# Kernel optimization log

Measured on AMD Instinct MI355X. Metric: run time of the kernel, lower is better.

## Reference

```python
import jax, jax.numpy as jnp
import numpy as np

BS, SL, H, DH = 2, 2048, 32, 128
STRIDE = 16
NUM_PAGES = BS * (SL // STRIDE)  # 256, distinct page per block
PAGE_DIM = 1 * 2 * STRIDE * H * DH  # blocks * partitions * stride * kv_heads * head_dim


def setup_inputs() -> dict:
    key = jax.random.key(0)
    k1, k2, k3 = jax.random.split(key, 3)
    xq = jax.random.normal(k1, (BS, SL, H, DH), dtype=jnp.float32)
    xk = jax.random.normal(k2, (BS, SL, H, DH), dtype=jnp.float32)
    xv = jax.random.normal(k3, (BS, SL, H, DH), dtype=jnp.float32)
    cache_state = jnp.zeros((NUM_PAGES, PAGE_DIM), dtype=jnp.float32)
    seq_block_ids = jnp.arange(BS * (SL // STRIDE), dtype=jnp.int64 if jax.config.jax_enable_x64 else jnp.int32).reshape(BS, SL // STRIDE)
    return {"xq": xq, "xk": xk, "xv": xv, "cache_state": cache_state, "seq_block_ids": seq_block_ids}


def reference(xq, xk, xv, cache_state, seq_block_ids):
    bs, sl, h, dh = xq.shape
    nb = sl // STRIDE  # blocks per sequence
    num_pages = cache_state.shape[0]

    # --- paged cache write (prefill path: start_positions is None) ---
    # page layout: [page, transformer_block(=1), partition(k=0,v=1), stride, head, head_dim]
    cache = cache_state.reshape(num_pages, 1, 2, STRIDE, h, dh)
    pids = seq_block_ids.reshape(-1)  # [bs*nb]
    k_blocks = xk.reshape(bs * nb, STRIDE, h, dh)
    v_blocks = xv.reshape(bs * nb, STRIDE, h, dh)
    cache = cache.at[pids, 0, 0].set(k_blocks)
    cache = cache.at[pids, 0, 1].set(v_blocks)
    new_cache_state = cache.reshape(cache_state.shape)

    # --- GQA repeat_kv: n_rep = head_count // head_count_kv = 1 -> no-op ---

    # --- SDPA, attn_mask=None, is_causal=False ---
    scale = 1.0 / np.sqrt(dh).astype(np.float32)
    scores = jnp.einsum("bqhd,bkhd->bhqk", xq, xk) * scale  # [bs, h, sl, sl]
    attn = jax.nn.softmax(scores, axis=-1)
    out = jnp.einsum("bhqk,bkhd->bqhd", attn, xv)
    attn_output = out.reshape(bs, sl, h * dh)
    return attn_output, new_cache_state
```

## Files before the change

### kernel.cpp

```cpp
#include <hip/hip_runtime.h>
#include <hip/hip_bf16.h>
#include <stdint.h>

#define BS 2
#define SL 2048
#define H 32
#define DH 128
#define ATT_ELEMS (BS*SL*H*DH)
#define KTILES (SL/64)
#define KT32 (SL/32)
#define QSCALE (0.08838834764831845f * 1.4426950408889634f)

typedef __attribute__((ext_vector_type(8))) short short8_t;
typedef __attribute__((ext_vector_type(16))) float f32x16_t;
typedef __attribute__((ext_vector_type(4))) unsigned int u32x4_t;
typedef __attribute__((ext_vector_type(2))) unsigned int u32x2_t;

union FragU { u32x4_t u; short8_t s; };

__device__ __forceinline__ unsigned short f2bf(float x){
    union { float f; unsigned int u; } v; v.f = x;
    unsigned int r = v.u + 0x7fffu + ((v.u >> 16) & 1u);
    return (unsigned short)(r >> 16);
}
__device__ __forceinline__ unsigned int pack2(float a, float b){
    return (unsigned int)f2bf(a) | ((unsigned int)f2bf(b) << 16);
}
__device__ __forceinline__ unsigned int cvtpk(float a, float b){
    unsigned int r;
    asm("v_cvt_pk_bf16_f32 %0, %1, %2" : "=v"(r) : "v"(a), "v"(b));
    return r;
}
__device__ __forceinline__ void gload16(const unsigned short* g, unsigned short* l){
    __builtin_amdgcn_global_load_lds(
        (const __attribute__((address_space(1))) void*)(const void*)g,
        (__attribute__((address_space(3))) void*)(void*)l, 16, 0, 0);
}

__global__ __launch_bounds__(256) void prep_kv_kernel(const float* __restrict__ xk,
                                                      const float* __restrict__ xv,
                                                      const int* __restrict__ pids,
                                                      unsigned short* __restrict__ kfr,
                                                      unsigned short* __restrict__ vfr,
                                                      float* __restrict__ out_cache,
                                                      int do_cache){
    __shared__ unsigned short tK[64*136];
    __shared__ unsigned short tV[64*136];
    int tile = blockIdx.x, h = blockIdx.y, b = blockIdx.z;
    int tid = threadIdx.x;
    size_t tb = ((size_t)((b*H + h)*KTILES + tile)) * 8192;
    int pg[4];
    #pragma unroll
    for (int j = 0; j < 4; ++j) pg[j] = pids[b*128 + tile*4 + j];

    #pragma unroll
    for (int i = 0; i < 8; ++i){
        int c = tid + 256*i;
        int row = c >> 5, f4 = c & 31;
        size_t gidx = ((size_t)((b*SL + tile*64 + row)*H + h))*DH + f4*4;
        float4 kx = *(const float4*)(xk + gidx);
        float4 vx = *(const float4*)(xv + gidx);
        u32x2_t kw; kw[0] = pack2(kx.x, kx.y); kw[1] = pack2(kx.z, kx.w);
        u32x2_t vw; vw[0] = pack2(vx.x, vx.y); vw[1] = pack2(vx.z, vx.w);
        *(u32x2_t*)(&tK[row*136 + f4*4]) = kw;
        *(u32x2_t*)(&tV[row*136 + f4*4]) = vw;
        if (do_cache){
            size_t cb = (size_t)pg[row>>4]*131072 + (size_t)(row&15)*4096 + h*128 + f4*4;
            *(float4*)(out_cache + cb)         = kx;
            *(float4*)(out_cache + cb + 65536) = vx;
        }
    }
    __syncthreads();
    #pragma unroll
    for (int i = 0; i < 4; ++i){
        int c = tid + 256*i;
        int sub = c >> 9, c2 = c & 511;
        int fi = c2 >> 6, l = c2 & 63;
        int key = sub*32 + (l & 31);
        int d0  = fi*16 + (l >> 5)*8;
        u32x4_t w = *(const u32x4_t*)(&tK[key*136 + d0]);
        *(u32x4_t*)(&kfr[tb + (size_t)sub*4096 + (size_t)c2*8]) = w;
    }
    #pragma unroll
    for (int i = 0; i < 4; ++i){
        int c = tid + 256*i;
        int sub = c >> 9, c2 = c & 511;
        int fi = c2 >> 6, l = c2 & 63;
        int d  = (fi >> 1)*32 + (l & 31);
        int k0 = sub*32 + (fi & 1)*16 + (l >> 5)*8;
        u32x4_t u;
        #pragma unroll
        for (int w = 0; w < 4; ++w)
            u[w] = (unsigned)tV[(k0+2*w)*136 + d] | ((unsigned)tV[(k0+2*w+1)*136 + d] << 16);
        *(u32x4_t*)(&vfr[tb + (size_t)sub*4096 + (size_t)c2*8]) = u;
    }
}

__global__ __launch_bounds__(256) void cache_scatter_kernel(const float* __restrict__ xk,
                                                            const float* __restrict__ xv,
                                                            const int* __restrict__ pids,
                                                            float* __restrict__ out_cache){
    int sb = blockIdx.x >> 1, part = blockIdx.x & 1;
    int page = pids[sb];
    const float4* s4 = (const float4*)((part ? xv : xk) + (size_t)sb * 65536);
    float4* d4 = (float4*)(out_cache + (size_t)page * 131072 + (size_t)part * 65536);
    int base = blockIdx.y * 2048 + threadIdx.x;
    #pragma unroll
    for (int i = 0; i < 8; ++i) d4[base + i*256] = s4[base + i*256];
}

__global__ __launch_bounds__(256, 3) void attn_kernel(const float* __restrict__ xq,
                                                      const unsigned short* __restrict__ kfr,
                                                      const unsigned short* __restrict__ vfr,
                                                      float* __restrict__ out){
    __shared__ unsigned short smem[4*4096];

    const int tid  = threadIdx.x;
    const int lane = tid & 63;
    const int wave = tid >> 6;
    const int l31  = lane & 31;
    const int hi   = lane >> 5;

    int lin = blockIdx.x;
    int swz = (lin & 7)*128 + (lin >> 3);
    const int qblk = swz & 15;
    const int h    = (swz >> 4) & 31;
    const int b    = swz >> 9;
    const int qbase = qblk*128 + wave*32;

    short8_t qf[8];
    {
        const float* qptr = xq + ((size_t)((b*SL + qbase + l31)*H + h))*DH + hi*8;
        #pragma unroll
        for (int f = 0; f < 8; ++f){
            float4 a = *(const float4*)(qptr + f*16);
            float4 c = *(const float4*)(qptr + f*16 + 4);
            FragU w;
            w.u[0] = pack2(a.x*QSCALE, a.y*QSCALE);
            w.u[1] = pack2(a.z*QSCALE, a.w*QSCALE);
            w.u[2] = pack2(c.x*QSCALE, c.y*QSCALE);
            w.u[3] = pack2(c.z*QSCALE, c.w*QSCALE);
            qf[f] = w.s;
        }
    }

    f32x16_t acc[4];
    #pragma unroll
    for (int d = 0; d < 4; ++d)
        #pragma unroll
        for (int r = 0; r < 16; ++r) acc[d][r] = 0.f;
    float m = -1e30f, l_run = 0.f;

    const size_t bh = (size_t)(b*H + h) * ((size_t)KT32*4096);
    const unsigned short* kg = kfr + bh;
    const unsigned short* vg = vfr + bh;

    #pragma unroll
    for (int i = 0; i < 2; ++i){
        int ch = wave*2 + i;
        gload16(kg + ch*512 + lane*8, smem + ch*512);
        gload16(vg + ch*512 + lane*8, smem + 8192 + ch*512);
    }
    asm volatile("s_waitcnt vmcnt(0)" ::: "memory");
    __builtin_amdgcn_s_barrier();
    asm volatile("" ::: "memory");

    #pragma unroll 1
    for (int t = 0; t < KT32; ++t){
        const int p = t & 1;
        unsigned short* Kc = smem + p*4096;
        unsigned short* Vc = smem + 8192 + p*4096;

        if (t + 1 < KT32){
            const unsigned short* kn = kg + (size_t)(t+1)*4096;
            const unsigned short* vn = vg + (size_t)(t+1)*4096;
            unsigned short* Kn = smem + (p^1)*4096;
            unsigned short* Vn = smem + 8192 + (p^1)*4096;
            #pragma unroll
            for (int i = 0; i < 2; ++i){
                int ch = wave*2 + i;
                gload16(kn + ch*512 + lane*8, Kn + ch*512);
                gload16(vn + ch*512 + lane*8, Vn + ch*512);
            }
        }
        __builtin_amdgcn_sched_barrier(0);

        f32x16_t sa, sb;
        #pragma unroll
        for (int r = 0; r < 16; ++r){ sa[r] = 0.f; sb[r] = 0.f; }
        __builtin_amdgcn_s_setprio(1);
        #pragma unroll
        for (int f = 0; f < 4; ++f){
            FragU k0, k1;
            k0.u = *(const u32x4_t*)(&Kc[(f  )*512 + lane*8]);
            k1.u = *(const u32x4_t*)(&Kc[(4+f)*512 + lane*8]);
            sa = __builtin_amdgcn_mfma_f32_32x32x16_bf16(k0.s, qf[f],   sa, 0, 0, 0);
            sb = __builtin_amdgcn_mfma_f32_32x32x16_bf16(k1.s, qf[4+f], sb, 0, 0, 0);
        }
        __builtin_amdgcn_s_setprio(0);
        f32x16_t s = sa + sb;

        float t8[8];
        #pragma unroll
        for (int r = 0; r < 8; ++r) t8[r] = fmaxf(s[r], s[8+r]);
        #pragma unroll
        for (int w = 4; w >= 1; w >>= 1)
            #pragma unroll
            for (int r = 0; r < 4; ++r)
                if (r < w) t8[r] = fmaxf(t8[r], t8[r+w]);
        float tmax = fmaxf(t8[0], __shfl_xor(t8[0], 32, 64));

        if (!__all(tmax - m <= 8.f)){
            float mn = fmaxf(m, tmax);
            float corr = __builtin_amdgcn_exp2f(m - mn);
            l_run *= corr;
            float cr[16];
            #pragma unroll
            for (int r = 0; r < 16; ++r)
                cr[r] = __shfl(corr, (r&3) + 8*(r>>2) + 4*hi, 64);
            #pragma unroll
            for (int d = 0; d < 4; ++d)
                #pragma unroll
                for (int r = 0; r < 16; ++r) acc[d][r] *= cr[r];
            m = mn;
        }

        float lsum = 0.f;
        FragU pf[2];
        #define PSLICE(KS, RB)                                                              \
        {                                                                                   \
            float e0 = __builtin_amdgcn_exp2f(s[RB+0] - m);                                 \
            float e1 = __builtin_amdgcn_exp2f(s[RB+1] - m);                                 \
            float e2 = __builtin_amdgcn_exp2f(s[RB+2] - m);                                 \
            float e3 = __builtin_amdgcn_exp2f(s[RB+3] - m);                                 \
            float e4 = __builtin_amdgcn_exp2f(s[RB+4] - m);                                 \
            float e5 = __builtin_amdgcn_exp2f(s[RB+5] - m);                                 \
            float e6 = __builtin_amdgcn_exp2f(s[RB+6] - m);                                 \
            float e7 = __builtin_amdgcn_exp2f(s[RB+7] - m);                                 \
            lsum += ((e0+e1)+(e2+e3)) + ((e4+e5)+(e6+e7));                                  \
            unsigned a  = cvtpk(e0,e1), bq = cvtpk(e2,e3);                                  \
            unsigned cq = cvtpk(e4,e5), dq = cvtpk(e6,e7);                                  \
            unsigned y0 = hi ? a : cq,  y1 = hi ? bq : dq;                                  \
            unsigned r0 = __shfl_xor(y0, 32, 64);                                           \
            unsigned r1 = __shfl_xor(y1, 32, 64);                                           \
            pf[KS].u[0] = hi ? r0 : a;  pf[KS].u[1] = hi ? r1 : bq;                         \
            pf[KS].u[2] = hi ? cq : r0; pf[KS].u[3] = hi ? dq : r1;                         \
        }
        PSLICE(0, 0)
        PSLICE(1, 8)
        #undef PSLICE
        lsum += __shfl_xor(lsum, 32, 64);
        l_run += lsum;

        __builtin_amdgcn_s_setprio(1);
        #pragma unroll
        for (int dblk = 0; dblk < 4; ++dblk){
            #pragma unroll
            for (int ks = 0; ks < 2; ++ks){
                FragU vb;
                vb.u = *(const u32x4_t*)(&Vc[(dblk*2 + ks)*512 + lane*8]);
                acc[dblk] = __builtin_amdgcn_mfma_f32_32x32x16_bf16(pf[ks].s, vb.s, acc[dblk], 0, 0, 0);
            }
        }
        __builtin_amdgcn_s_setprio(0);

        if (t + 1 < KT32){
            asm volatile("s_waitcnt vmcnt(0)" ::: "memory");
            __builtin_amdgcn_s_barrier();
            asm volatile("" ::: "memory");
        }
    }

    float linv = 1.f / l_run;
    float lr[16];
    #pragma unroll
    for (int r = 0; r < 16; ++r)
        lr[r] = __shfl(linv, (r&3) + 8*(r>>2) + 4*hi, 64);
    #pragma unroll
    for (int dblk = 0; dblk < 4; ++dblk){
        #pragma unroll
        for (int r = 0; r < 16; ++r){
            int q = qbase + (r&3) + 8*(r>>2) + 4*hi;
            out[(size_t)(b*SL + q)*(H*DH) + h*DH + dblk*32 + l31] = acc[dblk][r] * lr[r];
        }
    }
}

extern "C" void kernel_launch(void* const* d_in, const int* in_sizes, int n_in,
                              void* d_out, int out_size, void* d_ws, size_t ws_size,
                              hipStream_t stream) {
    const float* xq = (const float*)d_in[0];
    const float* xk = (const float*)d_in[1];
    const float* xv = (const float*)d_in[2];
    const int* pids = (const int*)d_in[4];

    float* out_attn  = (float*)d_out;
    float* out_cache = out_attn + (size_t)ATT_ELEMS;

    const size_t frag_elems = (size_t)BS*H*KTILES*8192;
    const size_t need       = 2*frag_elems*sizeof(unsigned short);

    if (ws_size >= need){
        unsigned short* kfr = (unsigned short*)d_ws;
        unsigned short* vfr = kfr + frag_elems;
        prep_kv_kernel<<<dim3(KTILES, H, BS), 256, 0, stream>>>(xk, xv, pids, kfr, vfr, out_cache, 1);
        attn_kernel<<<dim3(BS*H*(SL/128)), 256, 0, stream>>>(xq, kfr, vfr, out_attn);
    } else {
        unsigned short* vfr = (unsigned short*)out_cache;
        unsigned short* kfr = vfr + frag_elems;
        prep_kv_kernel<<<dim3(KTILES, H, BS), 256, 0, stream>>>(xk, xv, pids, kfr, vfr, out_cache, 0);
        attn_kernel<<<dim3(BS*H*(SL/128)), 256, 0, stream>>>(xq, kfr, vfr, out_attn);
        cache_scatter_kernel<<<dim3(512, 8), 256, 0, stream>>>(xk, xv, pids, out_cache);
    }
}
```

Measured before the change: 244.9 us.

## Software-pipeline QK^T one tile ahead of softmax and PV in attention

Restructures the attention loop so the QK^T MFMAs for tile t+1 are issued before the softmax and PV of tile t, letting matrix work overlap the exp/shuffle work. K is prefetched two tiles ahead and V one tile ahead, and a prologue computes the first score tile. The extra live score registers come with a launch-bounds occupancy hint lowered from 3 to 2 blocks per CU, trading occupancy for in-wave ILP.

```diff
diff --git a/kernel.cpp b/kernel.cpp
--- a/kernel.cpp
+++ b/kernel.cpp
@@ -109,7 +109,7 @@
     for (int i = 0; i < 8; ++i) d4[base + i*256] = s4[base + i*256];
 }
 
-__global__ __launch_bounds__(256, 3) void attn_kernel(const float* __restrict__ xq,
+__global__ __launch_bounds__(256, 2) void attn_kernel(const float* __restrict__ xq,
                                                       const unsigned short* __restrict__ kfr,
                                                       const unsigned short* __restrict__ vfr,
                                                       float* __restrict__ out){
@@ -158,51 +158,64 @@
     #pragma unroll
     for (int i = 0; i < 2; ++i){
         int ch = wave*2 + i;
-        gload16(kg + ch*512 + lane*8, smem + ch*512);
-        gload16(vg + ch*512 + lane*8, smem + 8192 + ch*512);
+        gload16(kg + ch*512 + lane*8,        smem + ch*512);
+        gload16(vg + ch*512 + lane*8,        smem + 8192 + ch*512);
+        gload16(kg + 4096 + ch*512 + lane*8, smem + 4096 + ch*512);
     }
     asm volatile("s_waitcnt vmcnt(0)" ::: "memory");
     __builtin_amdgcn_s_barrier();
     asm volatile("" ::: "memory");
 
+    f32x16_t s_prev;
+    #pragma unroll
+    for (int r = 0; r < 16; ++r) s_prev[r] = 0.f;
+    #pragma unroll
+    for (int f = 0; f < 8; ++f){
+        FragU kf; kf.u = *(const u32x4_t*)(&smem[f*512 + lane*8]);
+        s_prev = __builtin_amdgcn_mfma_f32_32x32x16_bf16(kf.s, qf[f], s_prev, 0, 0, 0);
+    }
+    __builtin_amdgcn_s_barrier();
+    asm volatile("" ::: "memory");
+
     #pragma unroll 1
     for (int t = 0; t < KT32; ++t){
         const int p = t & 1;
-        unsigned short* Kc = smem + p*4096;
-        unsigned short* Vc = smem + 8192 + p*4096;
-
-        if (t + 1 < KT32){
-            const unsigned short* kn = kg + (size_t)(t+1)*4096;
-            const unsigned short* vn = vg + (size_t)(t+1)*4096;
-            unsigned short* Kn = smem + (p^1)*4096;
-            unsigned short* Vn = smem + 8192 + (p^1)*4096;
+
+        if (t + 2 < KT32){
+            const unsigned short* kn = kg + (size_t)(t+2)*4096;
             #pragma unroll
             for (int i = 0; i < 2; ++i){
                 int ch = wave*2 + i;
-                gload16(kn + ch*512 + lane*8, Kn + ch*512);
-                gload16(vn + ch*512 + lane*8, Vn + ch*512);
+                gload16(kn + ch*512 + lane*8, smem + p*4096 + ch*512);
             }
         }
+        if (t + 1 < KT32){
+            const unsigned short* vn = vg + (size_t)(t+1)*4096;
+            #pragma unroll
+            for (int i = 0; i < 2; ++i){
+                int ch = wave*2 + i;
+                gload16(vn + ch*512 + lane*8, smem + 8192 + (p^1)*4096 + ch*512);
+            }
+        }
         __builtin_amdgcn_sched_barrier(0);
 
-        f32x16_t sa, sb;
-        #pragma unroll
-        for (int r = 0; r < 16; ++r){ sa[r] = 0.f; sb[r] = 0.f; }
         __builtin_amdgcn_s_setprio(1);
-        #pragma unroll
-        for (int f = 0; f < 4; ++f){
-            FragU k0, k1;
-            k0.u = *(const u32x4_t*)(&Kc[(f  )*512 + lane*8]);
-            k1.u = *(const u32x4_t*)(&Kc[(4+f)*512 + lane*8]);
-            sa = __builtin_amdgcn_mfma_f32_32x32x16_bf16(k0.s, qf[f],   sa, 0, 0, 0);
-            sb = __builtin_amdgcn_mfma_f32_32x32x16_bf16(k1.s, qf[4+f], sb, 0, 0, 0);
-        }
-        __builtin_amdgcn_s_setprio(0);
-        f32x16_t s = sa + sb;
+
+        f32x16_t s_new;
+        if (t + 1 < KT32){
+            #pragma unroll
+            for (int r = 0; r < 16; ++r) s_new[r] = 0.f;
+            const unsigned short* Kc = smem + (p^1)*4096;
+            #pragma unroll
+            for (int f = 0; f < 8; ++f){
+                FragU kf; kf.u = *(const u32x4_t*)(&Kc[f*512 + lane*8]);
+                s_new = __builtin_amdgcn_mfma_f32_32x32x16_bf16(kf.s, qf[f], s_new, 0, 0, 0);
+            }
+        }
 
         float t8[8];
         #pragma unroll
-        for (int r = 0; r < 8; ++r) t8[r] = fmaxf(s[r], s[8+r]);
+        for (int r = 0; r < 8; ++r) t8[r] = fmaxf(s_prev[r], s_prev[8+r]);
         #pragma unroll
         for (int w = 4; w >= 1; w >>= 1)
             #pragma unroll
@@ -229,14 +242,14 @@
         FragU pf[2];
         #define PSLICE(KS, RB)                                                              \
         {                                                                                   \
-            float e0 = __builtin_amdgcn_exp2f(s[RB+0] - m);                                 \
-            float e1 = __builtin_amdgcn_exp2f(s[RB+1] - m);                                 \
-            float e2 = __builtin_amdgcn_exp2f(s[RB+2] - m);                                 \
-            float e3 = __builtin_amdgcn_exp2f(s[RB+3] - m);                                 \
-            float e4 = __builtin_amdgcn_exp2f(s[RB+4] - m);                                 \
-            float e5 = __builtin_amdgcn_exp2f(s[RB+5] - m);                                 \
-            float e6 = __builtin_amdgcn_exp2f(s[RB+6] - m);                                 \
-            float e7 = __builtin_amdgcn_exp2f(s[RB+7] - m);                                 \
+            float e0 = __builtin_amdgcn_exp2f(s_prev[RB+0] - m);                            \
+            float e1 = __builtin_amdgcn_exp2f(s_prev[RB+1] - m);                            \
+            float e2 = __builtin_amdgcn_exp2f(s_prev[RB+2] - m);                            \
+            float e3 = __builtin_amdgcn_exp2f(s_prev[RB+3] - m);                            \
+            float e4 = __builtin_amdgcn_exp2f(s_prev[RB+4] - m);                            \
+            float e5 = __builtin_amdgcn_exp2f(s_prev[RB+5] - m);                            \
+            float e6 = __builtin_amdgcn_exp2f(s_prev[RB+6] - m);                            \
+            float e7 = __builtin_amdgcn_exp2f(s_prev[RB+7] - m);                            \
             lsum += ((e0+e1)+(e2+e3)) + ((e4+e5)+(e6+e7));                                  \
             unsigned a  = cvtpk(e0,e1), bq = cvtpk(e2,e3);                                  \
             unsigned cq = cvtpk(e4,e5), dq = cvtpk(e6,e7);                                  \
@@ -252,14 +265,16 @@
         lsum += __shfl_xor(lsum, 32, 64);
         l_run += lsum;
 
-        __builtin_amdgcn_s_setprio(1);
-        #pragma unroll
-        for (int dblk = 0; dblk < 4; ++dblk){
-            #pragma unroll
-            for (int ks = 0; ks < 2; ++ks){
-                FragU vb;
-                vb.u = *(const u32x4_t*)(&Vc[(dblk*2 + ks)*512 + lane*8]);
-                acc[dblk] = __builtin_amdgcn_mfma_f32_32x32x16_bf16(pf[ks].s, vb.s, acc[dblk], 0, 0, 0);
+        {
+            const unsigned short* Vc = smem + 8192 + p*4096;
+            #pragma unroll
+            for (int dblk = 0; dblk < 4; ++dblk){
+                #pragma unroll
+                for (int ks = 0; ks < 2; ++ks){
+                    FragU vb;
+                    vb.u = *(const u32x4_t*)(&Vc[(dblk*2 + ks)*512 + lane*8]);
+                    acc[dblk] = __builtin_amdgcn_mfma_f32_32x32x16_bf16(pf[ks].s, vb.s, acc[dblk], 0, 0, 0);
+                }
             }
         }
         __builtin_amdgcn_s_setprio(0);
@@ -268,6 +283,7 @@
             asm volatile("s_waitcnt vmcnt(0)" ::: "memory");
             __builtin_amdgcn_s_barrier();
             asm volatile("" ::: "memory");
+            s_prev = s_new;
         }
     }
 
```

Measured after the change: 246.6 us. No clear change (+0.7%).
